# Performance work log

Hardware: AMD Instinct MI355X
Metric: run time of the kernel (lower is better)

## Reference

```python
import jax, jax.numpy as jnp
import numpy as np

N = 50000      # n_nodes
E = 800000     # directed edges (symmetric set, no self-loops)
D_IN = 128
D_HID = 128
EPS = 1e-5     # LayerNorm eps (torch default)


def setup_inputs() -> dict:
    rng = np.random.default_rng(0)
    a = rng.integers(0, N, 700000, dtype=np.int64)
    b = rng.integers(0, N, 700000, dtype=np.int64)
    m = a != b
    a, b = a[m], b[m]
    # symmetric, deduplicated edge set (no self-loops); shuffle before truncation
    keys = np.unique(np.concatenate([a * N + b, b * N + a]))
    keys = rng.permutation(keys)[:E]
    row = (keys // N).astype(np.int32)
    col = (keys % N).astype(np.int32)
    ks = jax.random.split(jax.random.key(0), 6)
    return {
        "x": jax.random.normal(ks[0], (N, D_IN), jnp.float32),
        "W0": jax.random.normal(ks[1], (D_IN, D_HID), jnp.float32) / np.float32(np.sqrt(D_IN)),
        "b0": jnp.zeros((D_HID,), jnp.float32),
        "W1": jax.random.normal(ks[2], (D_HID, D_HID), jnp.float32) / np.float32(np.sqrt(D_HID)),
        "b1": jnp.zeros((D_HID,), jnp.float32),
        "ln1_g": jnp.ones((D_HID,), jnp.float32),
        "ln1_b": jnp.zeros((D_HID,), jnp.float32),
        "ln2_g": jnp.ones((D_HID,), jnp.float32),
        "ln2_b": jnp.zeros((D_HID,), jnp.float32),
        "drop_W": jax.random.normal(ks[3], (1, 2), jnp.float32) * 10.0,
        "drop_b": jnp.zeros((1,), jnp.float32),
        "row": jnp.asarray(row),
        "col": jnp.asarray(col),
    }


def _layernorm(h, g, b):
    mu = jnp.mean(h, axis=-1, keepdims=True)
    var = jnp.var(h, axis=-1, keepdims=True)
    return (h - mu) * jax.lax.rsqrt(var + EPS) * g + b


def _att_coef(h, row, col, drop_W, drop_b):
    # fused on-device version of the CPU att_coef: per-edge cosine sim,
    # threshold, row-l1-normalize, learned binary drop, self-loop lam, exp.
    n = h.shape[0]
    norms = jnp.sqrt(jnp.sum(h * h, axis=1))                      # [n]
    sim = jnp.sum(h[row] * h[col], axis=1) / (norms[row] * norms[col])  # [E]
    sim = jnp.where(sim < 0.1, 0.0, sim)
    rs = jax.ops.segment_sum(sim, row, num_segments=n)            # row l1 norms
    att = sim / jnp.where(rs[row] > 0, rs[row], 1.0)
    # reverse-edge lookup att[col,row] via sorted uint32 keys (n*n < 2**32)
    nn = jnp.uint32(n)
    keys = row.astype(jnp.uint32) * nn + col.astype(jnp.uint32)
    order = jnp.argsort(keys)
    sk = keys[order]
    rk = col.astype(jnp.uint32) * nn + row.astype(jnp.uint32)
    pos = jnp.clip(jnp.searchsorted(sk, rk), 0, keys.shape[0] - 1)
    att_rev = jnp.where(sk[pos] == rk, att[order[pos]], 0.0)
    # drop_learn: Linear(2,1) -> sigmoid -> Threshold(0.5,0) -> Threshold(-0.49,1)
    # net effect: binary mask = 1 if sigmoid(score) > 0.5 else 0
    score = jax.nn.sigmoid(att * drop_W[0, 0] + att_rev * drop_W[0, 1] + drop_b[0])
    att = att * (score > 0.5).astype(h.dtype)
    deg = jax.ops.segment_sum((att != 0).astype(h.dtype), row, num_segments=n)
    lam = 1.0 / (deg + 1.0)                                       # self-loop weight
    w_e = jnp.where(att != 0, jnp.exp(att), 0.0)                  # exp only on stored nnz
    w_diag = jnp.exp(lam)
    # original computes attention on CPU numpy -> detached from autograd
    return jax.lax.stop_gradient(w_e), jax.lax.stop_gradient(w_diag)


def _conv(h, w_e, w_diag, row, col, W, b):
    s = h @ W                                                      # [n, d_out]
    agg = jax.ops.segment_sum(w_e[:, None] * s[col], row, num_segments=h.shape[0])
    return agg + w_diag[:, None] * s + b


def reference(x, W0, b0, W1, b1, ln1_g, ln1_b, ln2_g, ln2_b, drop_W, drop_b, row, col):
    h = x
    # layer 0
    w_e, w_d = _att_coef(h, row, col, drop_W, drop_b)
    h = _conv(h, w_e, w_d, row, col, W0, b0)
    h = jax.nn.relu(_layernorm(h, ln1_g, ln1_b))   # dropout: eval mode -> identity
    # layer 1
    w_e, w_d = _att_coef(h, row, col, drop_W, drop_b)
    h = _conv(h, w_e, w_d, row, col, W1, b1)
    h = jax.nn.relu(_layernorm(h, ln2_g, ln2_b))
    # final block: source bug reuses the last loop conv (convs[-2] == W1,b1)
    w_e, w_d = _att_coef(h, row, col, drop_W, drop_b)
    h = _conv(h, w_e, w_d, row, col, W1, b1)
    return jax.nn.log_softmax(h, axis=-1)
```

## Files before the change

### kernel.cpp

```cpp
#include <hip/hip_runtime.h>
#include <hip/hip_bf16.h>

#define D 128
#define EPS 1e-5f
#define SCAP 32
#define GB 10

__global__ __launch_bounds__(256) void k_pre(
    const int* __restrict__ row, int* __restrict__ cnt, int E,
    const float* __restrict__ h, float* __restrict__ nrm, int N, int cB) {
  if ((int)blockIdx.x < cB) {
    int e = blockIdx.x * 256 + threadIdx.x;
    if (e < E) atomicAdd(&cnt[row[e]], 1);
  } else {
    int i = (blockIdx.x - cB) * 8 + (threadIdx.x >> 5);
    int sub = threadIdx.x & 31;
    if (i >= N) return;
    float4 a = ((const float4*)(h + (size_t)i * D))[sub];
    float v = a.x * a.x + a.y * a.y + a.z * a.z + a.w * a.w;
    for (int off = 16; off > 0; off >>= 1) v += __shfl_down(v, off, 32);
    if (sub == 0) nrm[i] = sqrtf(v);
  }
}

__global__ __launch_bounds__(256) void k_bsum(const int* __restrict__ cnt,
                                              int* __restrict__ bsum) {
  int t = threadIdx.x;
  int base = blockIdx.x * 1024 + t * 4;
  int4 c4 = ((const int4*)(cnt + base))[0];
  int s = c4.x + c4.y + c4.z + c4.w;
  for (int off = 32; off > 0; off >>= 1) s += __shfl_down(s, off);
  __shared__ int sh[4];
  if ((t & 63) == 0) sh[t >> 6] = s;
  __syncthreads();
  if (t == 0) bsum[blockIdx.x] = sh[0] + sh[1] + sh[2] + sh[3];
}

__global__ __launch_bounds__(256) void k_bscan(const int* __restrict__ bsum,
                                               int* __restrict__ boff, int nb,
                                               int* __restrict__ rptr, int N, int E) {
  __shared__ int sh[256];
  int t = threadIdx.x;
  int v = (t < nb) ? bsum[t] : 0;
  sh[t] = v;
  __syncthreads();
  for (int off = 1; off < 256; off <<= 1) {
    int u = (t >= off) ? sh[t - off] : 0;
    __syncthreads();
    sh[t] += u;
    __syncthreads();
  }
  if (t < nb) boff[t] = sh[t] - v;
  if (t == 0) rptr[N] = E;
}

__global__ __launch_bounds__(256) void k_apply(const int* __restrict__ cnt,
                                               const int* __restrict__ boff,
                                               int* __restrict__ rptr, int N) {
  __shared__ int sh[256];
  int t = threadIdx.x;
  int base = blockIdx.x * 1024 + t * 4;
  int4 c4 = ((const int4*)(cnt + base))[0];
  int e1 = c4.x, e2 = c4.x + c4.y, e3 = c4.x + c4.y + c4.z;
  int tot = e3 + c4.w;
  sh[t] = tot;
  __syncthreads();
  for (int off = 1; off < 256; off <<= 1) {
    int u = (t >= off) ? sh[t - off] : 0;
    __syncthreads();
    sh[t] += u;
    __syncthreads();
  }
  int o = sh[t] - tot + boff[blockIdx.x];
  if (base + 0 < N) rptr[base + 0] = o;
  if (base + 1 < N) rptr[base + 1] = o + e1;
  if (base + 2 < N) rptr[base + 2] = o + e2;
  if (base + 3 < N) rptr[base + 3] = o + e3;
}

__global__ __launch_bounds__(256) void k_bktA(
    const int* __restrict__ row, const int* __restrict__ col,
    const int* __restrict__ rptr, int* __restrict__ bcur,
    unsigned* __restrict__ pairs, int E) {
  int e = blockIdx.x * 256 + threadIdx.x;
  if (e < E) {
    int r = row[e];
    int b = r >> 7;
    int q = rptr[b << 7] + atomicAdd(&bcur[b * 16], 1);
    pairs[q] = ((unsigned)(r & 127) << 25) | (unsigned)col[e];
  }
}

__global__ __launch_bounds__(256) void k_bktB(
    const unsigned* __restrict__ pairs, const int* __restrict__ rptr,
    int* __restrict__ colS, int N) {
  __shared__ int curL[128];
  int b = blockIdx.x;
  int r0 = b << 7;
  int rend = min(r0 + 128, N);
  int q0 = rptr[r0], q1 = rptr[rend];
  if (threadIdx.x < 128) curL[threadIdx.x] = 0;
  __syncthreads();
  for (int q = q0 + threadIdx.x; q < q1; q += 256) {
    unsigned pk = pairs[q];
    int lr = pk >> 25;
    int c = (int)(pk & 0x1FFFFFFu);
    int p = rptr[r0 + lr] + atomicAdd(&curL[lr], 1);
    colS[p] = c;
  }
}

__global__ __launch_bounds__(256) void k_rev(const int* __restrict__ colS,
                                             const int* __restrict__ rptr,
                                             int* __restrict__ rev, int N) {
  int grp = threadIdx.x >> 5, sub = threadIdx.x & 31;
  int i = blockIdx.x * 8 + grp;
  if (i >= N) return;
  int p0 = rptr[i], p1 = rptr[i + 1];
  for (int p = p0 + sub; p < p1; p += 32) {
    int c = colS[p];
    int q1 = rptr[c + 1];
    int rv = -1;
    for (int q = rptr[c]; q < q1; ++q)
      if (colS[q] == i) { rv = q; break; }
    rev[p] = rv;
  }
}

__global__ __launch_bounds__(256) void k_sim(
    const float* __restrict__ h, const float* __restrict__ nrm,
    const int* __restrict__ rptr, const int* __restrict__ colS,
    const int* __restrict__ rev, float* __restrict__ simS, int N) {
  __shared__ int cL[8 * SCAP];
  __shared__ int pL[8 * SCAP];
  __shared__ int rL[8 * SCAP];
  __shared__ float nL[8 * SCAP];
  int grp = threadIdx.x >> 5;
  int sub = threadIdx.x & 31;
  int half = grp & 1;
  int i = blockIdx.x * 8 + grp;
  if (i >= N) return;
  int gb = grp * SCAP;
  int p0 = rptr[i], p1 = rptr[i + 1];
  float4 ai = ((const float4*)(h + (size_t)i * D))[sub];
  float ni = nrm[i];
  for (int base = p0; base < p1; base += SCAP) {
    int p = base + sub;
    bool inr = p < p1;
    int c = inr ? colS[p] : 0;
    int rv = inr ? rev[p] : 0;
    bool ok = inr && (c > i || rv < 0);
    unsigned long long mb = __ballot(ok);
    unsigned mh = (unsigned)(mb >> (half * 32));
    int pos = __popc(mh & ((1u << sub) - 1u));
    int K = __popc(mh);
    if (ok) {
      cL[gb + pos] = c;
      pL[gb + pos] = p;
      rL[gb + pos] = rv;
      nL[gb + pos] = nrm[c];
    }
    __builtin_amdgcn_wave_barrier();
    for (int j0 = 0; j0 < K; j0 += GB) {
      int cc_[GB];
      bool vv[GB];
      float4 b[GB];
#pragma unroll
      for (int k = 0; k < GB; ++k) {
        int idx = j0 + k;
        vv[k] = idx < K;
        cc_[k] = vv[k] ? cL[gb + idx] : i;
      }
#pragma unroll
      for (int k = 0; k < GB; ++k)
        b[k] = ((const float4*)(h + (size_t)cc_[k] * D))[sub];
#pragma unroll
      for (int k = 0; k < GB; ++k) {
        float v = ai.x * b[k].x + ai.y * b[k].y + ai.z * b[k].z + ai.w * b[k].w;
        for (int off = 16; off > 0; off >>= 1) v += __shfl_down(v, off, 32);
        if (sub == 0 && vv[k]) {
          int idx = j0 + k;
          float sm = v / (ni * nL[gb + idx]);
          sm = (sm < 0.1f) ? 0.0f : sm;
          simS[pL[gb + idx]] = sm;
          int rv2 = rL[gb + idx];
          if (rv2 >= 0) simS[rv2] = sm;
        }
      }
    }
    __builtin_amdgcn_wave_barrier();
  }
}

__global__ __launch_bounds__(256) void k_rs(const float* __restrict__ simS,
                                            const int* __restrict__ rptr,
                                            float* __restrict__ rsE, int N) {
  int i = blockIdx.x * 256 + threadIdx.x;
  if (i >= N) return;
  int p1 = rptr[i + 1];
  float rs = 0.f;
  for (int p = rptr[i]; p < p1; ++p) rs += simS[p];
  rsE[i] = (rs > 0.f) ? rs : 1.f;
}

__global__ __launch_bounds__(256) void k_gemm(const float* __restrict__ h,
                                              const float* __restrict__ W,
                                              float* __restrict__ S, int N) {
  __shared__ float Ws[64 * D];
  int t = threadIdx.x;
  int i0 = blockIdx.x * 64;
  int tx = t & 15, ty = t >> 4;
  int gi[4];
  bool vld[4];
#pragma unroll
  for (int r = 0; r < 4; ++r) {
    gi[r] = i0 + ty * 4 + r;
    vld[r] = gi[r] < N;
  }
  float acc[4][8] = {};
  for (int ph = 0; ph < 2; ++ph) {
    __syncthreads();
    for (int ch = 0; ch < 8; ++ch) {
      int q = t + 256 * ch;
      ((float4*)Ws)[q] = ((const float4*)(W + (size_t)ph * 64 * D))[q];
    }
    __syncthreads();
    for (int kk = 0; kk < 16; ++kk) {
      float4 a4[4];
#pragma unroll
      for (int r = 0; r < 4; ++r)
        a4[r] = vld[r] ? ((const float4*)(h + (size_t)gi[r] * D))[ph * 16 + kk]
                       : make_float4(0.f, 0.f, 0.f, 0.f);
      float4 b0[4], b1[4];
#pragma unroll
      for (int k = 0; k < 4; ++k) {
        b0[k] = ((const float4*)(Ws + (kk * 4 + k) * D))[tx];
        b1[k] = ((const float4*)(Ws + (kk * 4 + k) * D))[16 + tx];
      }
#pragma unroll
      for (int r = 0; r < 4; ++r) {
        float4 a = a4[r];
#pragma unroll
        for (int c = 0; c < 4; ++c) {
          acc[r][c] += a.x * (&b0[0].x)[c] + a.y * (&b0[1].x)[c] +
                       a.z * (&b0[2].x)[c] + a.w * (&b0[3].x)[c];
          acc[r][4 + c] += a.x * (&b1[0].x)[c] + a.y * (&b1[1].x)[c] +
                           a.z * (&b1[2].x)[c] + a.w * (&b1[3].x)[c];
        }
      }
    }
  }
#pragma unroll
  for (int r = 0; r < 4; ++r) {
    if (vld[r]) {
      ((float4*)(S + (size_t)gi[r] * D))[tx] =
          make_float4(acc[r][0], acc[r][1], acc[r][2], acc[r][3]);
      ((float4*)(S + (size_t)gi[r] * D))[16 + tx] =
          make_float4(acc[r][4], acc[r][5], acc[r][6], acc[r][7]);
    }
  }
}

template <int MODE>
__global__ __launch_bounds__(256) void k_combine(
    const float* __restrict__ s, const float* __restrict__ simS,
    const float* __restrict__ rsE, const int* __restrict__ rev,
    const int* __restrict__ rptr, const int* __restrict__ colS,
    const float* __restrict__ bias, const float* __restrict__ g,
    const float* __restrict__ be, const float* __restrict__ dWp,
    const float* __restrict__ dbp, float* __restrict__ outF,
    float* __restrict__ nrmOut, int N) {
  __shared__ float wL[8 * 32];
  __shared__ int cLd[8 * 32];
  int grp = threadIdx.x >> 5, sub = threadIdx.x & 31;
  int half = grp & 1;
  int i = blockIdx.x * 8 + grp;
  if (i >= N) return;
  int gb = grp * 32;
  float w0 = dWp[0], w1 = dWp[1], bd = dbp[0];
  int p0 = rptr[i], p1 = rptr[i + 1];
  float ri = rsE[i];
  float4 acc = make_float4(0.f, 0.f, 0.f, 0.f);
  int deg = 0;
  for (int base = p0; base < p1; base += 32) {
    int p = base + sub;
    bool inr = p < p1;
    float sm = inr ? simS[p] : 0.f;
    int c = inr ? colS[p] : 0;
    int rv = inr ? rev[p] : -1;
    bool keep = false;
    float a = 0.f;
    if (sm != 0.f) {
      a = sm / ri;
      float ar = (rv >= 0) ? sm / rsE[c] : 0.f;
      float x = a * w0 + ar * w1 + bd;
      float sc = (x >= 0.f) ? 1.f / (1.f + expf(-x)) : expf(x) / (1.f + expf(x));
      keep = sc > 0.5f;
    }
    unsigned long long mb = __ballot(keep);
    unsigned mh = (unsigned)(mb >> (half * 32));
    int pos = __popc(mh & ((1u << sub) - 1u));
    int K = __popc(mh);
    if (keep) {
      wL[gb + pos] = expf(a);
      cLd[gb + pos] = c;
    }
    __builtin_amdgcn_wave_barrier();
    deg += K;
    for (int j0 = 0; j0 < K; j0 += 8) {
      int cc_[8];
      float ww[8];
      float4 b[8];
#pragma unroll
      for (int k = 0; k < 8; ++k) {
        int idx = j0 + k;
        bool vv = idx < K;
        cc_[k] = vv ? cLd[gb + idx] : i;
        ww[k] = vv ? wL[gb + idx] : 0.f;
      }
#pragma unroll
      for (int k = 0; k < 8; ++k)
        b[k] = ((const float4*)(s + (size_t)cc_[k] * D))[sub];
#pragma unroll
      for (int k = 0; k < 8; ++k) {
        acc.x += ww[k] * b[k].x; acc.y += ww[k] * b[k].y;
        acc.z += ww[k] * b[k].z; acc.w += ww[k] * b[k].w;
      }
    }
    __builtin_amdgcn_wave_barrier();
  }
  float wd = expf(1.0f / (float)(deg + 1));
  float4 sv = ((const float4*)(s + (size_t)i * D))[sub];
  float4 bb = ((const float4*)bias)[sub];
  float4 v = make_float4(acc.x + wd * sv.x + bb.x, acc.y + wd * sv.y + bb.y,
                         acc.z + wd * sv.z + bb.z, acc.w + wd * sv.w + bb.w);
  if (MODE == 0) {
    float sm = v.x + v.y + v.z + v.w;
    for (int off = 16; off > 0; off >>= 1) sm += __shfl_down(sm, off, 32);
    float mu = __shfl(sm, 0, 32) * (1.f / 128.f);
    float4 dv = make_float4(v.x - mu, v.y - mu, v.z - mu, v.w - mu);
    float q = dv.x * dv.x + dv.y * dv.y + dv.z * dv.z + dv.w * dv.w;
    for (int off = 16; off > 0; off >>= 1) q += __shfl_down(q, off, 32);
    float var = __shfl(q, 0, 32) * (1.f / 128.f);
    float rstd = rsqrtf(var + EPS);
    float4 gg = ((const float4*)g)[sub];
    float4 eb = ((const float4*)be)[sub];
    float4 y = make_float4(fmaxf(dv.x * rstd * gg.x + eb.x, 0.f),
                           fmaxf(dv.y * rstd * gg.y + eb.y, 0.f),
                           fmaxf(dv.z * rstd * gg.z + eb.z, 0.f),
                           fmaxf(dv.w * rstd * gg.w + eb.w, 0.f));
    ((float4*)(outF + (size_t)i * D))[sub] = y;
    float q2 = y.x * y.x + y.y * y.y + y.z * y.z + y.w * y.w;
    for (int off = 16; off > 0; off >>= 1) q2 += __shfl_down(q2, off, 32);
    if (sub == 0) nrmOut[i] = sqrtf(q2);
  } else {
    float mx = fmaxf(fmaxf(v.x, v.y), fmaxf(v.z, v.w));
    for (int off = 16; off > 0; off >>= 1) mx = fmaxf(mx, __shfl_down(mx, off, 32));
    float m = __shfl(mx, 0, 32);
    float es = expf(v.x - m) + expf(v.y - m) + expf(v.z - m) + expf(v.w - m);
    for (int off = 16; off > 0; off >>= 1) es += __shfl_down(es, off, 32);
    float l = logf(__shfl(es, 0, 32)) + m;
    ((float4*)(outF + (size_t)i * D))[sub] =
        make_float4(v.x - l, v.y - l, v.z - l, v.w - l);
  }
}

extern "C" void kernel_launch(void* const* d_in, const int* in_sizes, int n_in,
                              void* d_out, int out_size, void* d_ws, size_t ws_size,
                              hipStream_t stream) {
  const float* x   = (const float*)d_in[0];
  const float* W0  = (const float*)d_in[1];
  const float* b0  = (const float*)d_in[2];
  const float* W1  = (const float*)d_in[3];
  const float* b1  = (const float*)d_in[4];
  const float* g1  = (const float*)d_in[5];
  const float* be1 = (const float*)d_in[6];
  const float* g2  = (const float*)d_in[7];
  const float* be2 = (const float*)d_in[8];
  const float* dW  = (const float*)d_in[9];
  const float* db  = (const float*)d_in[10];
  const int* row   = (const int*)d_in[11];
  const int* col   = (const int*)d_in[12];
  int N = in_sizes[0] / D;
  int E = in_sizes[11];
  float* out = (float*)d_out;

  float* base = (float*)d_ws;
  size_t off = 0;
  auto alloc = [&](size_t elems) {
    float* p = base + off;
    off += (elems + 3) & ~(size_t)3;
    return p;
  };
  size_t N128 = (size_t)N * D;
  int nb = (N + 1023) / 1024;
  int NpadS = nb * 1024;
  float* hA   = alloc(N128);
  float* hB   = alloc(N128);
  float* s    = alloc(N128);
  int*   colS = (int*)alloc(E);
  int*   rev  = (int*)alloc(E);
  float* simS = alloc(E);
  unsigned* pairs = (unsigned*)alloc(E);
  int*   cc   = (int*)alloc((size_t)2 * NpadS);
  int*   cnt  = cc;
  int*   bcur = cc + NpadS;
  int*   rptr = (int*)alloc(N + 1);
  float* rsE  = alloc(N);
  float* nrm  = alloc(N);
  int*   bsum = (int*)alloc(nb);
  int*   boff = (int*)alloc(nb);
  (void)ws_size; (void)n_in; (void)out_size;

  int cB = (E + 255) / 256;
  int nB = (N + 7) / 8;
  int nG = (N + 63) / 64;
  int nSim = (N + 7) / 8;
  int nRs = (N + 255) / 256;
  int nC = (N + 7) / 8;
  int NBKT = (N + 127) / 128;

  hipMemsetAsync(cc, 0, (size_t)2 * NpadS * sizeof(int), stream);
  k_pre<<<cB + nB, 256, 0, stream>>>(row, cnt, E, x, nrm, N, cB);
  k_bsum<<<nb, 256, 0, stream>>>(cnt, bsum);
  k_bscan<<<1, 256, 0, stream>>>(bsum, boff, nb, rptr, N, E);
  k_apply<<<nb, 256, 0, stream>>>(cnt, boff, rptr, N);
  k_bktA<<<cB, 256, 0, stream>>>(row, col, rptr, bcur, pairs, E);
  k_bktB<<<NBKT, 256, 0, stream>>>(pairs, rptr, colS, N);
  k_rev<<<nSim, 256, 0, stream>>>(colS, rptr, rev, N);

  auto layer = [&](const float* hin, float* hout, const float* Wf,
                   const float* bf, const float* gf, const float* bef,
                   float* nrmOut, int mode) {
    k_sim<<<nSim, 256, 0, stream>>>(hin, nrm, rptr, colS, rev, simS, N);
    k_rs<<<nRs, 256, 0, stream>>>(simS, rptr, rsE, N);
    k_gemm<<<nG, 256, 0, stream>>>(hin, Wf, s, N);
    if (mode == 0)
      k_combine<0><<<nC, 256, 0, stream>>>(s, simS, rsE, rev, rptr, colS, bf, gf,
                                           bef, dW, db, hout, nrmOut, N);
    else
      k_combine<1><<<nC, 256, 0, stream>>>(s, simS, rsE, rev, rptr, colS, bf, gf,
                                           bef, dW, db, hout, nullptr, N);
  };
  layer(x, hA, W0, b0, g1, be1, nrm, 0);
  layer(hA, hB, W1, b1, g2, be2, nrm, 0);
  layer(hB, out, W1, b1, nullptr, nullptr, nullptr, 1);
}
```

Baseline: 612.5 us.

## Merge scan kernels, fuse row-sum into GEMM launch, finer bucket atomics

Replaces the three-kernel prefix scan (bsum, bscan, apply) with one single-block scan kernel. Each thread scans a contiguous chunk of row counts serially. The per-row similarity sum is folded into the GEMM launch as extra blocks, which removes one launch per layer. Edge bucketing now uses 4-row buckets instead of 128-row buckets to spread atomic contention. The single-block scan trades launch overhead for serial per-thread work on one CU.

New measurement: 641.2 us. 1.05x slower.

```diff
diff --git a/kernel.cpp b/kernel.cpp
--- a/kernel.cpp
+++ b/kernel.cpp
@@ -23,26 +23,18 @@
   }
 }
 
-__global__ __launch_bounds__(256) void k_bsum(const int* __restrict__ cnt,
-                                              int* __restrict__ bsum) {
-  int t = threadIdx.x;
-  int base = blockIdx.x * 1024 + t * 4;
-  int4 c4 = ((const int4*)(cnt + base))[0];
-  int s = c4.x + c4.y + c4.z + c4.w;
-  for (int off = 32; off > 0; off >>= 1) s += __shfl_down(s, off);
-  __shared__ int sh[4];
-  if ((t & 63) == 0) sh[t >> 6] = s;
-  __syncthreads();
-  if (t == 0) bsum[blockIdx.x] = sh[0] + sh[1] + sh[2] + sh[3];
-}
-
-__global__ __launch_bounds__(256) void k_bscan(const int* __restrict__ bsum,
-                                               int* __restrict__ boff, int nb,
-                                               int* __restrict__ rptr, int N, int E) {
+__global__ __launch_bounds__(256) void k_scan(const int* __restrict__ cnt,
+                                              int* __restrict__ rptr,
+                                              int N, int E, int C) {
   __shared__ int sh[256];
   int t = threadIdx.x;
-  int v = (t < nb) ? bsum[t] : 0;
-  sh[t] = v;
+  int base = t * C;
+  int s = 0;
+  for (int j = 0; j < C; j += 4) {
+    int4 c4 = ((const int4*)(cnt + base + j))[0];
+    s += c4.x + c4.y + c4.z + c4.w;
+  }
+  sh[t] = s;
   __syncthreads();
   for (int off = 1; off < 256; off <<= 1) {
     int u = (t >= off) ? sh[t - off] : 0;
@@ -50,32 +42,16 @@
     sh[t] += u;
     __syncthreads();
   }
-  if (t < nb) boff[t] = sh[t] - v;
+  int run = sh[t] - s;
+  for (int j = 0; j < C; j += 4) {
+    int4 c4 = ((const int4*)(cnt + base + j))[0];
+    int i0 = base + j;
+    if (i0 + 0 < N) rptr[i0 + 0] = run;  run += c4.x;
+    if (i0 + 1 < N) rptr[i0 + 1] = run;  run += c4.y;
+    if (i0 + 2 < N) rptr[i0 + 2] = run;  run += c4.z;
+    if (i0 + 3 < N) rptr[i0 + 3] = run;  run += c4.w;
+  }
   if (t == 0) rptr[N] = E;
-}
-
-__global__ __launch_bounds__(256) void k_apply(const int* __restrict__ cnt,
-                                               const int* __restrict__ boff,
-                                               int* __restrict__ rptr, int N) {
-  __shared__ int sh[256];
-  int t = threadIdx.x;
-  int base = blockIdx.x * 1024 + t * 4;
-  int4 c4 = ((const int4*)(cnt + base))[0];
-  int e1 = c4.x, e2 = c4.x + c4.y, e3 = c4.x + c4.y + c4.z;
-  int tot = e3 + c4.w;
-  sh[t] = tot;
-  __syncthreads();
-  for (int off = 1; off < 256; off <<= 1) {
-    int u = (t >= off) ? sh[t - off] : 0;
-    __syncthreads();
-    sh[t] += u;
-    __syncthreads();
-  }
-  int o = sh[t] - tot + boff[blockIdx.x];
-  if (base + 0 < N) rptr[base + 0] = o;
-  if (base + 1 < N) rptr[base + 1] = o + e1;
-  if (base + 2 < N) rptr[base + 2] = o + e2;
-  if (base + 3 < N) rptr[base + 3] = o + e3;
 }
 
 __global__ __launch_bounds__(256) void k_bktA(
@@ -85,8 +61,8 @@
   int e = blockIdx.x * 256 + threadIdx.x;
   if (e < E) {
     int r = row[e];
-    int b = r >> 7;
-    int q = rptr[b << 7] + atomicAdd(&bcur[b * 16], 1);
+    int b = r >> 2;
+    int q = rptr[b << 2] + atomicAdd(&bcur[b], 1);
     pairs[q] = ((unsigned)(r & 127) << 25) | (unsigned)col[e];
   }
 }
@@ -192,23 +168,22 @@
   }
 }
 
-__global__ __launch_bounds__(256) void k_rs(const float* __restrict__ simS,
-                                            const int* __restrict__ rptr,
-                                            float* __restrict__ rsE, int N) {
-  int i = blockIdx.x * 256 + threadIdx.x;
-  if (i >= N) return;
-  int p1 = rptr[i + 1];
-  float rs = 0.f;
-  for (int p = rptr[i]; p < p1; ++p) rs += simS[p];
-  rsE[i] = (rs > 0.f) ? rs : 1.f;
-}
-
-__global__ __launch_bounds__(256) void k_gemm(const float* __restrict__ h,
-                                              const float* __restrict__ W,
-                                              float* __restrict__ S, int N) {
+__global__ __launch_bounds__(256) void k_gemmrs(
+    const float* __restrict__ h, const float* __restrict__ W,
+    float* __restrict__ S, const float* __restrict__ simS,
+    const int* __restrict__ rptr, float* __restrict__ rsE, int N, int nG) {
   __shared__ float Ws[64 * D];
+  if ((int)blockIdx.x >= nG) {
+    int i = ((int)blockIdx.x - nG) * 256 + threadIdx.x;
+    if (i >= N) return;
+    int p1 = rptr[i + 1];
+    float rs = 0.f;
+    for (int p = rptr[i]; p < p1; ++p) rs += simS[p];
+    rsE[i] = (rs > 0.f) ? rs : 1.f;
+    return;
+  }
   int t = threadIdx.x;
-  int i0 = blockIdx.x * 64;
+  int i0 = (int)blockIdx.x * 64;
   int tx = t & 15, ty = t >> 4;
   int gi[4];
   bool vld[4];
@@ -408,8 +383,6 @@
   int*   rptr = (int*)alloc(N + 1);
   float* rsE  = alloc(N);
   float* nrm  = alloc(N);
-  int*   bsum = (int*)alloc(nb);
-  int*   boff = (int*)alloc(nb);
   (void)ws_size; (void)n_in; (void)out_size;
 
   int cB = (E + 255) / 256;
@@ -422,9 +395,7 @@
 
   hipMemsetAsync(cc, 0, (size_t)2 * NpadS * sizeof(int), stream);
   k_pre<<<cB + nB, 256, 0, stream>>>(row, cnt, E, x, nrm, N, cB);
-  k_bsum<<<nb, 256, 0, stream>>>(cnt, bsum);
-  k_bscan<<<1, 256, 0, stream>>>(bsum, boff, nb, rptr, N, E);
-  k_apply<<<nb, 256, 0, stream>>>(cnt, boff, rptr, N);
+  k_scan<<<1, 256, 0, stream>>>(cnt, rptr, N, E, nb * 4);
   k_bktA<<<cB, 256, 0, stream>>>(row, col, rptr, bcur, pairs, E);
   k_bktB<<<NBKT, 256, 0, stream>>>(pairs, rptr, colS, N);
   k_rev<<<nSim, 256, 0, stream>>>(colS, rptr, rev, N);
@@ -433,8 +404,7 @@
                    const float* bf, const float* gf, const float* bef,
                    float* nrmOut, int mode) {
     k_sim<<<nSim, 256, 0, stream>>>(hin, nrm, rptr, colS, rev, simS, N);
-    k_rs<<<nRs, 256, 0, stream>>>(simS, rptr, rsE, N);
-    k_gemm<<<nG, 256, 0, stream>>>(hin, Wf, s, N);
+    k_gemmrs<<<nG + nRs, 256, 0, stream>>>(hin, Wf, s, simS, rptr, rsE, N, nG);
     if (mode == 0)
       k_combine<0><<<nC, 256, 0, stream>>>(s, simS, rsE, rev, rptr, colS, bf, gf,
                                            bef, dW, db, hout, nrmOut, N);
```
